# Kernel tuning notes

Measured on AMD Instinct MI355X. Metric: run time of the kernel, lower is better.

## Reference

```python
import jax, jax.numpy as jnp
import numpy as np

SEQ_LENGTH = 4096
HIDDEN = 4096
N_HEADS = 32
N_KV = 2
HEAD_DIM = 128
ROT_DIM = 64  # head_dim // 2, rotary applied to first half
FFN = 13696
EPS = 1e-5


def rope_cache(seq_len):
    theta = 1.0 / (10000.0 ** (jnp.arange(0, ROT_DIM, 2, dtype=jnp.float32) / ROT_DIM))  # [32]
    idx = jnp.arange(seq_len, dtype=jnp.float32)
    freqs = jnp.outer(idx, theta)  # [seq, 32]
    return jnp.stack([jnp.cos(freqs), jnp.sin(freqs)], axis=-1)  # [seq, 32, 2]


def apply_rope(x, rope):
    # x: [sq, b, nh, 128]; rope: [sq, b, 32, 2]
    sq, b, nh, hn = x.shape
    xr = x[..., :ROT_DIM].reshape(sq, b, nh, ROT_DIM // 2, 2)
    x0, x1 = xr[..., 0], xr[..., 1]
    cos = rope[:, :, None, :, 0]
    sin = rope[:, :, None, :, 1]
    out = jnp.stack([x0 * cos - x1 * sin, x1 * cos + x0 * sin], axis=-1)
    out = out.reshape(sq, b, nh, ROT_DIM)
    return jnp.concatenate([out, x[..., ROT_DIM:]], axis=-1)


def rmsnorm(x, w):
    var = jnp.mean(jnp.square(x), axis=-1, keepdims=True)
    return x * jax.lax.rsqrt(var + EPS) * w


def setup_inputs() -> dict:
    key = jax.random.key(0)
    ks = jax.random.split(key, 12)
    B, L = 32, SEQ_LENGTH - 1
    s = 0.02
    return {
        'hidden_states': jax.random.normal(ks[0], (1, B, HIDDEN), jnp.float32),
        'position_ids': jax.random.randint(ks[1], (B, 1), 0, SEQ_LENGTH),
        'attention_mask': jnp.zeros((B, 1, 1, SEQ_LENGTH), dtype=bool),
        'past_k': jax.random.normal(ks[2], (L, B, N_KV, HEAD_DIM), jnp.float32),
        'past_v': jax.random.normal(ks[3], (L, B, N_KV, HEAD_DIM), jnp.float32),
        'w_ln1': 1.0 + s * jax.random.normal(ks[4], (HIDDEN,), jnp.float32),
        'w_qkv': s * jax.random.normal(ks[5], (HIDDEN + 2 * N_KV * HEAD_DIM, HIDDEN), jnp.float32),
        'b_qkv': s * jax.random.normal(ks[6], (HIDDEN + 2 * N_KV * HEAD_DIM,), jnp.float32),
        'w_dense': s * jax.random.normal(ks[7], (HIDDEN, HIDDEN), jnp.float32),
        'w_ln2': 1.0 + s * jax.random.normal(ks[8], (HIDDEN,), jnp.float32),
        'w_fc1': s * jax.random.normal(ks[9], (2 * FFN, HIDDEN), jnp.float32),
        'w_fc2': s * jax.random.normal(ks[10], (HIDDEN, FFN), jnp.float32),
    }


def reference(hidden_states, position_ids, attention_mask, past_k, past_v,
              w_ln1, w_qkv, b_qkv, w_dense, w_ln2, w_fc1, w_fc2):
    sq, B, _ = hidden_states.shape
    # rotary_pos_emb(SEQ_LENGTH)[position_ids].transpose(0, 1)
    rope = rope_cache(SEQ_LENGTH)[position_ids]          # [B, sq, 32, 2]
    rope = jnp.transpose(rope, (1, 0, 2, 3))             # [sq, B, 32, 2]

    # --- self attention ---
    residual = hidden_states
    x = rmsnorm(hidden_states, w_ln1)
    qkv = jnp.einsum('sbh,oh->sbo', x, w_qkv) + b_qkv    # [sq, B, 4608]
    q = qkv[..., :HIDDEN].reshape(sq, B, N_HEADS, HEAD_DIM)
    k = qkv[..., HIDDEN:HIDDEN + N_KV * HEAD_DIM].reshape(sq, B, N_KV, HEAD_DIM)
    v = qkv[..., HIDDEN + N_KV * HEAD_DIM:].reshape(sq, B, N_KV, HEAD_DIM)
    q = apply_rope(q, rope)
    k = apply_rope(k, rope)

    k_cache = jnp.concatenate([past_k, k], axis=0)       # [L+sq, B, 2, 128]
    v_cache = jnp.concatenate([past_v, v], axis=0)

    rep = N_HEADS // N_KV
    kx = jnp.repeat(k_cache, rep, axis=2)                # [sk, B, 32, 128]
    vx = jnp.repeat(v_cache, rep, axis=2)

    scale = 1.0 / jnp.sqrt(jnp.float32(HEAD_DIM))
    scores = jnp.einsum('qbhd,kbhd->bhqk', q, kx) * scale  # [B, 32, sq, sk]
    scores = jnp.where(attention_mask, jnp.float32(-1e9), scores)
    probs = jax.nn.softmax(scores, axis=-1)
    ctx = jnp.einsum('bhqk,kbhd->qbhd', probs, vx).reshape(sq, B, HIDDEN)
    attn_out = jnp.einsum('sbh,oh->sbo', ctx, w_dense)

    hidden = residual + attn_out

    # --- MLP (SwiGLU) ---
    residual = hidden
    x = rmsnorm(hidden, w_ln2)
    h = jnp.einsum('sbh,oh->sbo', x, w_fc1)              # [sq, B, 2*FFN]
    a, b = jnp.split(h, 2, axis=-1)
    h = jax.nn.silu(a) * b
    mlp_out = jnp.einsum('sbf,of->sbo', h, w_fc2)
    hidden = residual + mlp_out

    return hidden, k_cache[1:], v_cache[1:]
```

## Files before the change

kernel.cpp:

```cpp
#include <hip/hip_runtime.h>


constexpr int B    = 32;
constexpr int HID  = 4096;
constexpr int NKV  = 2;
constexpr int HD   = 128;
constexpr int QKVN = 4608;
constexpr int FFN  = 13696;
constexpr int FC1N = 2 * FFN;
constexpr int PAST = 4095;
constexpr int NSPL = 16;

constexpr size_t OFF_X1   = 0;
constexpr size_t OFF_P    = OFF_X1   + (size_t)B * HID;
constexpr size_t P_SIZE   = 4ull * B * FC1N;
constexpr size_t OFF_Q    = OFF_P    + P_SIZE;
constexpr size_t OFF_KN   = OFF_Q    + (size_t)B * HID;
constexpr size_t OFF_VN   = OFF_KN   + (size_t)B * NKV * HD;
constexpr size_t OFF_CTXP = OFF_VN   + (size_t)B * NKV * HD;
constexpr size_t OFF_ML   = OFF_CTXP + (size_t)B * NKV * NSPL * 16 * HD;
constexpr size_t OFF_CTX  = OFF_ML   + (size_t)B * NKV * NSPL * 16 * 2;
constexpr size_t OFF_HID  = OFF_CTX  + (size_t)B * HID;
constexpr size_t OFF_X2   = OFF_HID  + (size_t)B * HID;
constexpr size_t OFF_HG   = OFF_X2   + (size_t)B * HID;

__global__ __launch_bounds__(256) void k_rmsnorm(
    const float* __restrict__ x, const float* __restrict__ w,
    float* __restrict__ out)
{
  const int b = blockIdx.x, t = threadIdx.x;
  const float* xr = x + (size_t)b * HID;
  float4 v[4];
  float ss = 0.f;
#pragma unroll
  for (int r = 0; r < 4; r++) {
    v[r] = *(const float4*)&xr[(t + r * 256) * 4];
    ss += v[r].x * v[r].x + v[r].y * v[r].y + v[r].z * v[r].z + v[r].w * v[r].w;
  }
#pragma unroll
  for (int off = 32; off; off >>= 1) ss += __shfl_xor(ss, off);
  __shared__ float wsum[4];
  if ((t & 63) == 0) wsum[t >> 6] = ss;
  __syncthreads();
  const float tot = wsum[0] + wsum[1] + wsum[2] + wsum[3];
  const float inv = rsqrtf(tot * (1.f / HID) + 1e-5f);
  float* orow = out + (size_t)b * HID;
#pragma unroll
  for (int r = 0; r < 4; r++) {
    const int i = (t + r * 256) * 4;
    const float4 wv = *(const float4*)&w[i];
    float4 o;
    o.x = v[r].x * inv * wv.x;
    o.y = v[r].y * inv * wv.y;
    o.z = v[r].z * inv * wv.z;
    o.w = v[r].w * inv * wv.w;
    *(float4*)&orow[i] = o;
  }
}

__global__ __launch_bounds__(256) void k_resid_norm(
    const float* __restrict__ hs, const float* __restrict__ dpart,
    const float* __restrict__ w, float* __restrict__ hid,
    float* __restrict__ out)
{
  const int b = blockIdx.x, t = threadIdx.x;
  float4 v[4];
  float ss = 0.f;
#pragma unroll
  for (int r = 0; r < 4; r++) {
    const int i = (t + r * 256) * 4;
    float4 a = *(const float4*)&hs[(size_t)b * HID + i];
#pragma unroll
    for (int s = 0; s < 16; s++) {
      const float4 p = *(const float4*)&dpart[((size_t)s * B + b) * HID + i];
      a.x += p.x; a.y += p.y; a.z += p.z; a.w += p.w;
    }
    v[r] = a;
    *(float4*)&hid[(size_t)b * HID + i] = a;
    ss += a.x * a.x + a.y * a.y + a.z * a.z + a.w * a.w;
  }
#pragma unroll
  for (int off = 32; off; off >>= 1) ss += __shfl_xor(ss, off);
  __shared__ float wsum[4];
  if ((t & 63) == 0) wsum[t >> 6] = ss;
  __syncthreads();
  const float tot = wsum[0] + wsum[1] + wsum[2] + wsum[3];
  const float inv = rsqrtf(tot * (1.f / HID) + 1e-5f);
#pragma unroll
  for (int r = 0; r < 4; r++) {
    const int i = (t + r * 256) * 4;
    const float4 wv = *(const float4*)&w[i];
    float4 o;
    o.x = v[r].x * inv * wv.x;
    o.y = v[r].y * inv * wv.y;
    o.z = v[r].z * inv * wv.z;
    o.w = v[r].w * inv * wv.w;
    *(float4*)&out[(size_t)b * HID + i] = o;
  }
}

__global__ __launch_bounds__(256, 2) void k_gemv32(
    const float* __restrict__ A, const float* __restrict__ W,
    const float* __restrict__ bias, float* __restrict__ outp,
    int N, int K, int ksplit_len)
{
  __shared__ __align__(16) float xs[8192];
  const int t = threadIdx.x;
  const int wv = t >> 6, l = t & 63;
  const int olane = l >> 3, kq = l & 7;
  const int o_base = blockIdx.x * 64;
  const int kb = blockIdx.y * ksplit_len;
  const int ke = kb + ksplit_len;

  float acc[8][8];
#pragma unroll
  for (int j = 0; j < 8; j++)
#pragma unroll
    for (int bb = 0; bb < 8; bb++) acc[j][bb] = 0.f;

  const float* W0 = W + (size_t)(o_base + olane) * K;
  const size_t rowstride8 = (size_t)8 * K;

  for (int kc = kb; kc < ke; kc += 256) {
    const int csz = min(256, ke - kc);
    const int c4n = csz >> 2;
    __syncthreads();
#pragma unroll
    for (int r = 0; r < 8; r++) {
      const int f = t + r * 256;
      const int b = f >> 6, c4 = f & 63;
      if (c4 < c4n)
        *(float4*)&xs[b * 256 + c4 * 4] =
            *(const float4*)&A[(size_t)b * K + kc + c4 * 4];
    }
    __syncthreads();
#pragma unroll
    for (int i = 0; i < 8; i++) {
      const int kl = i * 32 + kq * 4;
      if (kl < csz) {
        float4 w4[8];
#pragma unroll
        for (int j = 0; j < 8; j++)
          w4[j] = *(const float4*)&W0[j * rowstride8 + kc + kl];
#pragma unroll
        for (int bb = 0; bb < 8; bb++) {
          const float4 xv = *(const float4*)&xs[(wv * 8 + bb) * 256 + kl];
#pragma unroll
          for (int j = 0; j < 8; j++)
            acc[j][bb] += w4[j].x * xv.x + w4[j].y * xv.y +
                          w4[j].z * xv.z + w4[j].w * xv.w;
        }
      }
    }
  }
#pragma unroll
  for (int j = 0; j < 8; j++)
#pragma unroll
    for (int bb = 0; bb < 8; bb++) {
      float v = acc[j][bb];
      v += __shfl_xor(v, 1);
      v += __shfl_xor(v, 2);
      v += __shfl_xor(v, 4);
      acc[j][bb] = v;
    }
  __syncthreads();
  if (kq == 0) {
#pragma unroll
    for (int j = 0; j < 8; j++)
#pragma unroll
      for (int bb = 0; bb < 8; bb++)
        xs[(olane + 8 * j) * 33 + (wv * 8 + bb)] = acc[j][bb];
  }
  __syncthreads();
#pragma unroll
  for (int r = 0; r < 8; r++) {
    const int pair = t + r * 256;
    const int b = pair >> 6, rl = pair & 63;
    float v = xs[rl * 33 + b];
    if (bias != nullptr && blockIdx.y == 0) v += bias[o_base + rl];
    outp[((size_t)blockIdx.y * B + b) * N + o_base + rl] = v;
  }
}

__global__ __launch_bounds__(256) void k_qkv_rope(
    const float* __restrict__ qkvp, const int* __restrict__ pos_ids,
    float* __restrict__ qo, float* __restrict__ ko, float* __restrict__ vo)
{
  const int idx = blockIdx.x * 256 + threadIdx.x;
  const int b = idx / 1152;
  const int f4 = idx - b * 1152;
  const int o = f4 * 4;
  float4 v = {0.f, 0.f, 0.f, 0.f};
#pragma unroll
  for (int s = 0; s < 16; s++) {
    const float4 p = *(const float4*)&qkvp[((size_t)s * B + b) * QKVN + o];
    v.x += p.x; v.y += p.y; v.z += p.z; v.w += p.w;
  }
  const int d = o & 127;
  if (o < HID + NKV * HD && d < 64) {
    const int pos = pos_ids[b];
    const int i0 = d >> 1;
    const float f0 = pos * __expf(-0.28782313662425572f * i0);
    const float f1 = pos * __expf(-0.28782313662425572f * (i0 + 1));
    float c0, s0, c1, s1;
    sincosf(f0, &s0, &c0);
    sincosf(f1, &s1, &c1);
    float4 r;
    r.x = v.x * c0 - v.y * s0;
    r.y = v.y * c0 + v.x * s0;
    r.z = v.z * c1 - v.w * s1;
    r.w = v.w * c1 + v.z * s1;
    v = r;
  }
  if (o < HID) {
    *(float4*)&qo[(size_t)b * HID + o] = v;
  } else if (o < HID + NKV * HD) {
    *(float4*)&ko[(size_t)b * (NKV * HD) + (o - HID)] = v;
  } else {
    *(float4*)&vo[(size_t)b * (NKV * HD) + (o - HID - NKV * HD)] = v;
  }
}

__global__ __launch_bounds__(256) void k_attn_partial(
    const float* __restrict__ q, const float* __restrict__ past_k,
    const float* __restrict__ past_v, const float* __restrict__ kn,
    const float* __restrict__ vn, float* __restrict__ ok,
    float* __restrict__ ov, float* __restrict__ ctxp,
    float* __restrict__ mlbuf)
{
  __shared__ __align__(16) float smem[8192];
  float* sc = smem;
  float* qs = smem + 5120;
  const int t = threadIdx.x;
  const int split = blockIdx.x, kvh = blockIdx.y, b = blockIdx.z;

#pragma unroll
  for (int r = 0; r < 2; r++) {
    const int f4 = t + r * 256;
    const int hh = f4 >> 5, d4q = f4 & 31;
    *(float4*)&qs[hh * 128 + d4q * 4] =
        *(const float4*)&q[(size_t)b * HID + (kvh * 16 + hh) * HD + d4q * 4];
  }

  {
    const int r8 = t >> 5, d4c = t & 31;
#pragma unroll
    for (int g = 0; g < 4; g++) {
      float4 kv[8];
#pragma unroll
      for (int u = 0; u < 8; u++) {
        const int pg = split * 256 + (g * 8 + u) * 8 + r8;
        kv[u] = (pg < PAST)
            ? *(const float4*)&past_k[(((size_t)pg * B + b) * NKV + kvh) * HD + d4c * 4]
            : *(const float4*)&kn[((size_t)b * NKV + kvh) * HD + d4c * 4];
      }
#pragma unroll
      for (int u = 0; u < 8; u++) {
        const int pg = split * 256 + (g * 8 + u) * 8 + r8;
        if (pg >= 1)
          *(float4*)&ok[(((size_t)(pg - 1) * B + b) * NKV + kvh) * HD + d4c * 4] = kv[u];
      }
    }
  }
  __syncthreads();

  const float scale = 0.08838834764831845f;
  {
    const int pg = split * 256 + t;
    const float* kr = (pg < PAST)
        ? &past_k[(((size_t)pg * B + b) * NKV + kvh) * HD]
        : &kn[((size_t)b * NKV + kvh) * HD];
    float s[16];
#pragma unroll
    for (int hh = 0; hh < 16; hh++) s[hh] = 0.f;
#pragma unroll 4
    for (int d4 = 0; d4 < 32; d4++) {
      const float4 kv = *(const float4*)&kr[d4 * 4];
#pragma unroll
      for (int hh = 0; hh < 16; hh++) {
        const float4 q4 = *(const float4*)&qs[hh * 128 + d4 * 4];
        s[hh] += q4.x * kv.x + q4.y * kv.y + q4.z * kv.z + q4.w * kv.w;
      }
    }
#pragma unroll
    for (int hh = 0; hh < 16; hh++) sc[t * 20 + hh] = s[hh] * scale;
  }
  __syncthreads();

  {
    const int hh = t >> 4, l16 = t & 15;
    float m = -1e30f;
    for (int jj = 0; jj < 16; jj++)
      m = fmaxf(m, sc[(l16 + jj * 16) * 20 + hh]);
#pragma unroll
    for (int off = 8; off; off >>= 1) m = fmaxf(m, __shfl_xor(m, off));
    float lsum = 0.f;
    for (int jj = 0; jj < 16; jj++) {
      const int p = l16 + jj * 16;
      const float e = __expf(sc[p * 20 + hh] - m);
      sc[p * 20 + hh] = e;
      lsum += e;
    }
#pragma unroll
    for (int off = 8; off; off >>= 1) lsum += __shfl_xor(lsum, off);
    if (l16 == 0) {
      const size_t base =
          (((size_t)(b * NKV + kvh) * NSPL + split) * 16 + hh) * 2;
      mlbuf[base] = m;
      mlbuf[base + 1] = lsum;
    }
  }
  __syncthreads();

  const int pr = t >> 5, d4 = t & 31;
  float4 acc[16];
#pragma unroll
  for (int hh = 0; hh < 16; hh++) acc[hh] = float4{0.f, 0.f, 0.f, 0.f};
#pragma unroll
  for (int g = 0; g < 8; g++) {
    float4 v4[4];
#pragma unroll
    for (int u = 0; u < 4; u++) {
      const int pg = split * 256 + pr * 32 + g * 4 + u;
      v4[u] = (pg < PAST)
          ? *(const float4*)&past_v[(((size_t)pg * B + b) * NKV + kvh) * HD + d4 * 4]
          : *(const float4*)&vn[((size_t)b * NKV + kvh) * HD + d4 * 4];
    }
#pragma unroll
    for (int u = 0; u < 4; u++) {
      const int pg = split * 256 + pr * 32 + g * 4 + u;
      if (pg >= 1)
        *(float4*)&ov[(((size_t)(pg - 1) * B + b) * NKV + kvh) * HD + d4 * 4] = v4[u];
    }
#pragma unroll
    for (int u = 0; u < 4; u++) {
      const int pl = pr * 32 + g * 4 + u;
#pragma unroll
      for (int h4 = 0; h4 < 4; h4++) {
        const float4 e = *(const float4*)&sc[pl * 20 + h4 * 4];
        acc[h4 * 4 + 0].x += e.x * v4[u].x; acc[h4 * 4 + 0].y += e.x * v4[u].y;
        acc[h4 * 4 + 0].z += e.x * v4[u].z; acc[h4 * 4 + 0].w += e.x * v4[u].w;
        acc[h4 * 4 + 1].x += e.y * v4[u].x; acc[h4 * 4 + 1].y += e.y * v4[u].y;
        acc[h4 * 4 + 1].z += e.y * v4[u].z; acc[h4 * 4 + 1].w += e.y * v4[u].w;
        acc[h4 * 4 + 2].x += e.z * v4[u].x; acc[h4 * 4 + 2].y += e.z * v4[u].y;
        acc[h4 * 4 + 2].z += e.z * v4[u].z; acc[h4 * 4 + 2].w += e.z * v4[u].w;
        acc[h4 * 4 + 3].x += e.w * v4[u].x; acc[h4 * 4 + 3].y += e.w * v4[u].y;
        acc[h4 * 4 + 3].z += e.w * v4[u].z; acc[h4 * 4 + 3].w += e.w * v4[u].w;
      }
    }
  }
#pragma unroll
  for (int hh = 0; hh < 16; hh++) {
    acc[hh].x += __shfl_xor(acc[hh].x, 32);
    acc[hh].y += __shfl_xor(acc[hh].y, 32);
    acc[hh].z += __shfl_xor(acc[hh].z, 32);
    acc[hh].w += __shfl_xor(acc[hh].w, 32);
  }
  __syncthreads();
  if ((t & 63) < 32) {
    const int w = t >> 6;
#pragma unroll
    for (int hh = 0; hh < 16; hh++)
      *(float4*)&smem[w * 2048 + hh * 128 + d4 * 4] = acc[hh];
  }
  __syncthreads();
#pragma unroll
  for (int r = 0; r < 8; r++) {
    const int o = t + r * 256;
    const int hh = o >> 7, d = o & 127;
    const float v = smem[hh * 128 + d] + smem[2048 + hh * 128 + d] +
                    smem[4096 + hh * 128 + d] + smem[6144 + hh * 128 + d];
    ctxp[(((size_t)(b * NKV + kvh) * NSPL + split) * 16 + hh) * HD + d] = v;
  }
}

__global__ __launch_bounds__(128) void k_attn_merge(
    const float* __restrict__ ctxp, const float* __restrict__ mlbuf,
    float* __restrict__ ctx)
{
  const int h = blockIdx.x, b = blockIdx.y, d = threadIdx.x;
  const int kvh = h >> 4, hh = h & 15;
  float ms[NSPL], ls[NSPL];
  float M = -1e30f;
#pragma unroll
  for (int s = 0; s < NSPL; s++) {
    const size_t base = (((size_t)(b * NKV + kvh) * NSPL + s) * 16 + hh) * 2;
    ms[s] = mlbuf[base];
    ls[s] = mlbuf[base + 1];
    M = fmaxf(M, ms[s]);
  }
  float L = 0.f, val = 0.f;
#pragma unroll
  for (int s = 0; s < NSPL; s++) {
    const float w = __expf(ms[s] - M);
    L += ls[s] * w;
    val += w * ctxp[(((size_t)(b * NKV + kvh) * NSPL + s) * 16 + hh) * HD + d];
  }
  ctx[(size_t)b * HID + h * HD + d] = val / L;
}

__global__ __launch_bounds__(256) void k_swiglu(
    const float* __restrict__ h1p, float* __restrict__ hg)
{
  const int idx = blockIdx.x * 256 + threadIdx.x;
  const int b = idx / 3424;
  const int f4 = idx - b * 3424;
  float4 a = {0.f, 0.f, 0.f, 0.f}, g = {0.f, 0.f, 0.f, 0.f};
#pragma unroll
  for (int s = 0; s < 4; s++) {
    const float4 av = *(const float4*)&h1p[((size_t)s * B + b) * FC1N + f4 * 4];
    const float4 gv =
        *(const float4*)&h1p[((size_t)s * B + b) * FC1N + FFN + f4 * 4];
    a.x += av.x; a.y += av.y; a.z += av.z; a.w += av.w;
    g.x += gv.x; g.y += gv.y; g.z += gv.z; g.w += gv.w;
  }
  float4 o;
  o.x = a.x / (1.f + __expf(-a.x)) * g.x;
  o.y = a.y / (1.f + __expf(-a.y)) * g.y;
  o.z = a.z / (1.f + __expf(-a.z)) * g.z;
  o.w = a.w / (1.f + __expf(-a.w)) * g.w;
  *(float4*)&hg[(size_t)b * FFN + f4 * 4] = o;
}

__global__ __launch_bounds__(256) void k_final(
    const float* __restrict__ hid, const float* __restrict__ fp,
    float* __restrict__ out)
{
  const int idx = blockIdx.x * 256 + threadIdx.x;
  const int b = idx >> 10, i4 = idx & 1023;
  float4 v = *(const float4*)&hid[(size_t)b * HID + i4 * 4];
#pragma unroll
  for (int s = 0; s < 16; s++) {
    const float4 p = *(const float4*)&fp[((size_t)s * B + b) * HID + i4 * 4];
    v.x += p.x; v.y += p.y; v.z += p.z; v.w += p.w;
  }
  *(float4*)&out[(size_t)b * HID + i4 * 4] = v;
}

extern "C" void kernel_launch(void* const* d_in, const int* in_sizes, int n_in,
                              void* d_out, int out_size, void* d_ws,
                              size_t ws_size, hipStream_t stream)
{
  const float* hs     = (const float*)d_in[0];
  const int*   pos    = (const int*)  d_in[1];
  const float* pk     = (const float*)d_in[3];
  const float* pv     = (const float*)d_in[4];
  const float* wln1   = (const float*)d_in[5];
  const float* wqkv   = (const float*)d_in[6];
  const float* bqkv   = (const float*)d_in[7];
  const float* wdense = (const float*)d_in[8];
  const float* wln2   = (const float*)d_in[9];
  const float* wfc1   = (const float*)d_in[10];
  const float* wfc2   = (const float*)d_in[11];

  float* ws  = (float*)d_ws;
  float* out = (float*)d_out;

  float* x1    = ws + OFF_X1;
  float* P     = ws + OFF_P;
  float* q     = ws + OFF_Q;
  float* kn    = ws + OFF_KN;
  float* vn    = ws + OFF_VN;
  float* ctxp  = ws + OFF_CTXP;
  float* mlbuf = ws + OFF_ML;
  float* ctx   = ws + OFF_CTX;
  float* hid   = ws + OFF_HID;
  float* x2    = ws + OFF_X2;
  float* hg    = ws + OFF_HG;

  float* out_k = out + (size_t)B * HID;
  float* out_v = out_k + (size_t)PAST * B * NKV * HD;

  hipLaunchKernelGGL(k_rmsnorm, dim3(B), dim3(256), 0, stream, hs, wln1, x1);
  hipLaunchKernelGGL(k_gemv32, dim3(QKVN / 64, 16), dim3(256), 0, stream,
                     x1, wqkv, bqkv, P, QKVN, HID, HID / 16);
  hipLaunchKernelGGL(k_qkv_rope, dim3(144), dim3(256), 0, stream,
                     P, pos, q, kn, vn);
  hipLaunchKernelGGL(k_attn_partial, dim3(NSPL, NKV, B), dim3(256), 0, stream,
                     q, pk, pv, kn, vn, out_k, out_v, ctxp, mlbuf);
  hipLaunchKernelGGL(k_attn_merge, dim3(32, 32), dim3(128), 0, stream,
                     ctxp, mlbuf, ctx);
  hipLaunchKernelGGL(k_gemv32, dim3(HID / 64, 16), dim3(256), 0, stream,
                     ctx, wdense, (const float*)nullptr, P, HID, HID, HID / 16);
  hipLaunchKernelGGL(k_resid_norm, dim3(B), dim3(256), 0, stream,
                     hs, P, wln2, hid, x2);
  hipLaunchKernelGGL(k_gemv32, dim3(FC1N / 64, 4), dim3(256), 0, stream,
                     x2, wfc1, (const float*)nullptr, P, FC1N, HID, HID / 4);
  hipLaunchKernelGGL(k_swiglu, dim3(428), dim3(256), 0, stream, P, hg);
  hipLaunchKernelGGL(k_gemv32, dim3(HID / 64, 16), dim3(256), 0, stream,
                     hg, wfc2, (const float*)nullptr, P, HID, FFN, FFN / 16);
  hipLaunchKernelGGL(k_final, dim3(128), dim3(256), 0, stream, hid, P, out);
}
```

Baseline: 591.4 us.

## Split PV accumulation across head halves to cut registers and raise occupancy

The probability-times-V stage in the partial attention kernel now gives each thread 8 heads instead of 16, with the two halves of the block covering different head groups and each thread handling 64 positions. This halves the accumulator register footprint, and launch bounds now request 4 blocks per SM. The cross-wave reduction is simplified to one shared-memory exchange. In exchange, each V row is loaded twice (once per head half), while the cache copy-out is written only by the first half.

```diff
diff --git a/kernel.cpp b/kernel.cpp
--- a/kernel.cpp
+++ b/kernel.cpp
@@ -221,7 +221,7 @@
   }
 }
 
-__global__ __launch_bounds__(256) void k_attn_partial(
+__global__ __launch_bounds__(256, 4) void k_attn_partial(
     const float* __restrict__ q, const float* __restrict__ past_k,
     const float* __restrict__ past_v, const float* __restrict__ kn,
     const float* __restrict__ vn, float* __restrict__ ok,
@@ -312,32 +312,32 @@
   }
   __syncthreads();
 
-  const int pr = t >> 5, d4 = t & 31;
-  float4 acc[16];
-#pragma unroll
-  for (int hh = 0; hh < 16; hh++) acc[hh] = float4{0.f, 0.f, 0.f, 0.f};
+  const int d4 = t & 31, pq = (t >> 5) & 3, hp = t >> 7;
+  float4 acc[8];
+#pragma unroll
+  for (int hh = 0; hh < 8; hh++) acc[hh] = float4{0.f, 0.f, 0.f, 0.f};
 #pragma unroll
   for (int g = 0; g < 8; g++) {
-    float4 v4[4];
-#pragma unroll
-    for (int u = 0; u < 4; u++) {
-      const int pg = split * 256 + pr * 32 + g * 4 + u;
+    float4 v4[8];
+#pragma unroll
+    for (int u = 0; u < 8; u++) {
+      const int pg = split * 256 + pq * 64 + g * 8 + u;
       v4[u] = (pg < PAST)
           ? *(const float4*)&past_v[(((size_t)pg * B + b) * NKV + kvh) * HD + d4 * 4]
           : *(const float4*)&vn[((size_t)b * NKV + kvh) * HD + d4 * 4];
     }
 #pragma unroll
-    for (int u = 0; u < 4; u++) {
-      const int pg = split * 256 + pr * 32 + g * 4 + u;
-      if (pg >= 1)
+    for (int u = 0; u < 8; u++) {
+      const int pg = split * 256 + pq * 64 + g * 8 + u;
+      if (hp == 0 && pg >= 1)
         *(float4*)&ov[(((size_t)(pg - 1) * B + b) * NKV + kvh) * HD + d4 * 4] = v4[u];
     }
 #pragma unroll
-    for (int u = 0; u < 4; u++) {
-      const int pl = pr * 32 + g * 4 + u;
-#pragma unroll
-      for (int h4 = 0; h4 < 4; h4++) {
-        const float4 e = *(const float4*)&sc[pl * 20 + h4 * 4];
+    for (int u = 0; u < 8; u++) {
+      const int pl = pq * 64 + g * 8 + u;
+#pragma unroll
+      for (int h4 = 0; h4 < 2; h4++) {
+        const float4 e = *(const float4*)&sc[pl * 20 + hp * 8 + h4 * 4];
         acc[h4 * 4 + 0].x += e.x * v4[u].x; acc[h4 * 4 + 0].y += e.x * v4[u].y;
         acc[h4 * 4 + 0].z += e.x * v4[u].z; acc[h4 * 4 + 0].w += e.x * v4[u].w;
         acc[h4 * 4 + 1].x += e.y * v4[u].x; acc[h4 * 4 + 1].y += e.y * v4[u].y;
@@ -350,27 +350,30 @@
     }
   }
 #pragma unroll
-  for (int hh = 0; hh < 16; hh++) {
+  for (int hh = 0; hh < 8; hh++) {
     acc[hh].x += __shfl_xor(acc[hh].x, 32);
     acc[hh].y += __shfl_xor(acc[hh].y, 32);
     acc[hh].z += __shfl_xor(acc[hh].z, 32);
     acc[hh].w += __shfl_xor(acc[hh].w, 32);
   }
   __syncthreads();
-  if ((t & 63) < 32) {
-    const int w = t >> 6;
-#pragma unroll
-    for (int hh = 0; hh < 16; hh++)
-      *(float4*)&smem[w * 2048 + hh * 128 + d4 * 4] = acc[hh];
-  }
-  __syncthreads();
-#pragma unroll
-  for (int r = 0; r < 8; r++) {
-    const int o = t + r * 256;
-    const int hh = o >> 7, d = o & 127;
-    const float v = smem[hh * 128 + d] + smem[2048 + hh * 128 + d] +
-                    smem[4096 + hh * 128 + d] + smem[6144 + hh * 128 + d];
-    ctxp[(((size_t)(b * NKV + kvh) * NSPL + split) * 16 + hh) * HD + d] = v;
+  const int w = t >> 6;
+  if ((w & 1) == 1 && (t & 63) < 32) {
+#pragma unroll
+    for (int hh = 0; hh < 8; hh++)
+      *(float4*)&smem[hp * 1024 + hh * 128 + d4 * 4] = acc[hh];
+  }
+  __syncthreads();
+  if ((w & 1) == 0 && (t & 63) < 32) {
+    const size_t base =
+        (((size_t)(b * NKV + kvh) * NSPL + split) * 16 + hp * 8) * HD;
+#pragma unroll
+    for (int hh = 0; hh < 8; hh++) {
+      const float4 p = *(const float4*)&smem[hp * 1024 + hh * 128 + d4 * 4];
+      float4 o = acc[hh];
+      o.x += p.x; o.y += p.y; o.z += p.z; o.w += p.w;
+      *(float4*)&ctxp[base + (size_t)hh * HD + d4 * 4] = o;
+    }
   }
 }
 
```

After: 805.5 us. +36.2%, slower.
